# Kernel tuning notes

Hardware: AMD Instinct MI355X
Metric: run time of the kernel (lower is better)

The kernel has to match this reference:

```python
import jax, jax.numpy as jnp
import numpy as np

# T=timepoints, B=batch, N=neurons, H=lstm hidden, D=INPUT_DIM, P=len(PEOPLE)
T, B, N, H, D, P = 512, 64, 256, 64, 128, 64


def setup_inputs() -> dict:
    key = jax.random.key(0)
    ks = jax.random.split(key, 11)
    s = lambda k, shape, sc: jax.random.normal(k, shape, dtype=jnp.float32) * sc
    return {
        "input": s(ks[0], (T, B, D), 1.0),
        "W2n": s(ks[1], (N, D), D ** -0.5),      # linear2neurons weight [N, D]
        "b2n": s(ks[2], (N,), D ** -0.5),
        "W_ih": s(ks[3], (4 * H, 1), 1.0),        # LSTMCell input weights (input_size=1)
        "W_hh": s(ks[4], (4 * H, H), H ** -0.5),  # LSTMCell recurrent weights
        "b_ih": s(ks[5], (4 * H,), H ** -0.5),
        "b_hh": s(ks[6], (4 * H,), H ** -0.5),
        "Wg": s(ks[7], (1, H), H ** -0.5),        # linearLSTM: H -> 1 gain
        "bg": s(ks[8], (1,), H ** -0.5),
        "Wout": s(ks[9], (P, N), N ** -0.5),      # neurons2output
        "bout": s(ks[10], (P,), N ** -0.5),
    }


def reference(input, W2n, b2n, W_ih, W_hh, b_ih, b_hh, Wg, bg, Wout, bout):
    # Drive to every neuron for all timesteps: [T, B, N]
    x2n = jnp.einsum('tbd,nd->tbn', input, W2n) + b2n
    h0 = jnp.zeros((B, N, H), input.dtype)
    g0 = jnp.zeros((B, N), input.dtype)
    bias = b_ih + b_hh
    w_ih = W_ih[:, 0]  # [4H], since lstm input is scalar per neuron
    wg = Wg[0]         # [H]

    def step(carry, inp):
        h, c, g_prev1, g_prev2 = carry  # g_prev1 = g_{t-1}, g_prev2 = g_{t-2}
        xt, t = inp                     # xt: [B, N]
        # PyTorch LSTMCell gate order: i, f, g, o
        gates = xt[..., None] * w_ih + jnp.einsum('bnh,gh->bng', h, W_hh) + bias  # [B,N,4H]
        i_g, f_g, c_g, o_g = jnp.split(gates, 4, axis=-1)
        c = jax.nn.sigmoid(f_g) * c + jax.nn.sigmoid(i_g) * jnp.tanh(c_g)
        h = jax.nn.sigmoid(o_g) * jnp.tanh(c)
        g_t = jnp.einsum('bnh,h->bn', h, wg) + bg[0]  # gain at time t, [B,N]
        # original list semantics: t=0 uses g_t itself, t=1 uses constant 1, t>=2 uses g_{t-2}
        gain = jnp.where(t == 0, g_t, jnp.where(t == 1, jnp.ones_like(g_t), g_prev2))
        out = gain * jax.nn.softplus(xt - 1.0)  # log(1 + exp(x - 1))
        return (h, c, g_t, g_prev1), out

    _, out_neurons = jax.lax.scan(step, (h0, h0, g0, g0), (x2n, jnp.arange(T)))
    # out_neurons: [T, B, N] -> final projection to people logits [T, B, P]
    return jnp.einsum('tbn,pn->tbp', out_neurons, Wout) + bout
```

## Files before the change

### kernel.cpp

```cpp
#include <hip/hip_runtime.h>
#include <hip/hip_bf16.h>


typedef __attribute__((ext_vector_type(4))) float f32x4;
typedef __attribute__((ext_vector_type(4))) short s16x4;
typedef __attribute__((ext_vector_type(8))) short s16x8;
typedef __attribute__((ext_vector_type(4))) unsigned u32x4;

__device__ inline short bf16r(float f) {
    unsigned u = __builtin_bit_cast(unsigned, f);
    u += 0x7fffu + ((u >> 16) & 1u);
    return (short)(u >> 16);
}
__device__ inline float bf2f(short s) {
    unsigned u = ((unsigned)(unsigned short)s) << 16;
    return __builtin_bit_cast(float, u);
}
__device__ inline unsigned pkbf(float a, float b) {
    unsigned r;
    asm("v_cvt_pk_bf16_f32 %0, %1, %2" : "=v"(r) : "v"(a), "v"(b));
    return r;
}
__device__ inline f32x4 mfma32(s16x8 a, s16x8 b, f32x4 c) {
    return __builtin_amdgcn_mfma_f32_16x16x32_bf16(a, b, c, 0, 0, 0);
}

__global__ __launch_bounds__(256) void gemm_xwT(
    const float* __restrict__ X, const float* __restrict__ Wt,
    const float* __restrict__ bias, float* __restrict__ Out,
    int N, int K)
{
    __shared__ float Xs[32][68];
    __shared__ float Ws[32][68];
    const int tid = threadIdx.x;
    const int tx = tid & 15, ty = tid >> 4;
    const int m0 = blockIdx.x * 64, n0 = blockIdx.y * 64;
    const int kq = tid & 7, mr = tid >> 3;

    float acc[4][4];
#pragma unroll
    for (int i = 0; i < 4; ++i)
#pragma unroll
        for (int j = 0; j < 4; ++j) acc[i][j] = 0.f;

    for (int kc = 0; kc < K; kc += 32) {
#pragma unroll
        for (int rr = 0; rr < 2; ++rr) {
            const int m = mr + rr * 32;
            f32x4 xv = *(const f32x4*)(X + (size_t)(m0 + m) * K + kc + kq * 4);
            f32x4 wv = *(const f32x4*)(Wt + (size_t)(n0 + m) * K + kc + kq * 4);
#pragma unroll
            for (int j = 0; j < 4; ++j) { Xs[kq*4 + j][m] = xv[j]; Ws[kq*4 + j][m] = wv[j]; }
        }
        __syncthreads();
#pragma unroll
        for (int k = 0; k < 32; ++k) {
            f32x4 a = *(const f32x4*)&Xs[k][ty * 4];
            f32x4 b = *(const f32x4*)&Ws[k][tx * 4];
#pragma unroll
            for (int i = 0; i < 4; ++i)
#pragma unroll
                for (int j = 0; j < 4; ++j)
                    acc[i][j] = __builtin_fmaf(a[i], b[j], acc[i][j]);
        }
        __syncthreads();
    }
    f32x4 bv = *(const f32x4*)(bias + n0 + tx * 4);
#pragma unroll
    for (int i = 0; i < 4; ++i) {
        f32x4 o;
#pragma unroll
        for (int j = 0; j < 4; ++j) o[j] = acc[i][j] + bv[j];
        *(f32x4*)(Out + (size_t)(m0 + ty * 4 + i) * N + n0 + tx * 4) = o;
    }
}

__global__ __launch_bounds__(64, 1) void lstm_scan(
    const float* __restrict__ x2n,
    const float* __restrict__ W_hh,
    const float* __restrict__ w_ih,
    const float* __restrict__ b_ih,
    const float* __restrict__ b_hh,
    const float* __restrict__ wg,
    const float* __restrict__ bg,
    float* __restrict__ ON)
{
    const int lane = threadIdx.x & 63;
    const int c15 = lane & 15, g4 = lane >> 4;
    const int cellbase = blockIdx.x * 16;
    const float L2E = 1.4426950408889634f;

    s16x8 afw8[2][16];
    s16x8 afx8[16];
#pragma unroll
    for (int nt = 0; nt < 16; ++nt) {
        const float sc = ((nt >> 2) == 2) ? (2.f * L2E) : (-L2E);
        const float* wrow = W_hh + (size_t)(nt * 16 + c15) * 64;
#pragma unroll
        for (int kp = 0; kp < 2; ++kp) {
            s16x8 v;
#pragma unroll
            for (int half = 0; half < 2; ++half) {
                f32x4 w = *(const f32x4*)(wrow + (kp * 2 + half) * 16 + g4 * 4);
#pragma unroll
                for (int e = 0; e < 4; ++e) v[half * 4 + e] = bf16r(w[e] * sc);
            }
            afw8[kp][nt] = v;
        }
        const int g = nt * 16 + c15;
        const float wi = w_ih[g] * sc;
        const float bs = (b_ih[g] + b_hh[g]) * sc;
        const short wh = bf16r(wi);
        const short wl = bf16r(wi - bf2f(wh));
        const short bh_ = bf16r(bs);
        const short bl_ = bf16r(bs - bf2f(bh_));
        s16x8 v = (s16x8){0, 0, 0, 0, 0, 0, 0, 0};
        if (g4 == 0) { v[0] = wh; v[1] = wh; v[2] = wl; v[3] = bh_; }
        else if (g4 == 1) { v[0] = bl_; }
        afx8[nt] = v;
    }

    f32x4 wg_l[4];
#pragma unroll
    for (int q = 0; q < 4; ++q) wg_l[q] = *(const f32x4*)(wg + q * 16 + g4 * 4);
    const float bg0 = bg[0];
    const short one_bf = (short)0x3F80;

    f32x4 cst[4];
#pragma unroll
    for (int q = 0; q < 4; ++q) cst[q] = (f32x4){0.f, 0.f, 0.f, 0.f};
    s16x8 bh01 = (s16x8){0, 0, 0, 0, 0, 0, 0, 0};
    s16x8 bh23 = (s16x8){0, 0, 0, 0, 0, 0, 0, 0};

    float g_s1 = 0.f;
    float g2save = 0.f;
    float sp0 = 0.f;

    const size_t cellidx = (size_t)cellbase + c15;
    float xs0 = x2n[cellidx];
    float xs1 = x2n[(size_t)16384 + cellidx];

    for (int t = 0; t < 512; ++t) {
#pragma unroll
        for (int nt = 0; nt < 16; ++nt) {
            asm volatile("" : "+v"(afw8[0][nt]));
            asm volatile("" : "+v"(afw8[1][nt]));
            asm volatile("" : "+v"(afx8[nt]));
        }

        const float s2new = g_s1 + __shfl_xor(g_s1, 32, 64);

        const float xs_cur = xs0;
        xs0 = xs1;
        xs1 = x2n[(size_t)((t + 2) & 511) * 16384 + cellidx];

        const short xh = bf16r(xs_cur);
        const short xl = bf16r(xs_cur - bf2f(xh));
        s16x8 bx8 = (s16x8){0, 0, 0, 0, 0, 0, 0, 0};
        if (g4 == 0) { bx8[0] = xh; bx8[1] = xl; bx8[2] = xh; bx8[3] = one_bf; }
        else if (g4 == 1) { bx8[0] = one_bf; }

        unsigned bhw[8];
        float gpart = 0.f;
        const f32x4 zero4 = (f32x4){0.f, 0.f, 0.f, 0.f};
#pragma unroll
        for (int q = 0; q < 4; ++q) {
            f32x4 ai = mfma32(afx8[q], bx8, zero4);
            f32x4 af_ = mfma32(afx8[q + 4], bx8, zero4);
            f32x4 ag_ = mfma32(afx8[q + 8], bx8, zero4);
            f32x4 ao_ = mfma32(afx8[q + 12], bx8, zero4);
            ai  = mfma32(afw8[0][q], bh01, ai);       ai  = mfma32(afw8[1][q], bh23, ai);
            af_ = mfma32(afw8[0][q + 4], bh01, af_);  af_ = mfma32(afw8[1][q + 4], bh23, af_);
            ag_ = mfma32(afw8[0][q + 8], bh01, ag_);  ag_ = mfma32(afw8[1][q + 8], bh23, ag_);
            ao_ = mfma32(afw8[0][q + 12], bh01, ao_); ao_ = mfma32(afw8[1][q + 12], bh23, ao_);

            f32x4 hv;
#pragma unroll
            for (int ep = 0; ep < 2; ++ep) {
                const int ea = 2 * ep, eb = ea + 1;
                const float ufa = __builtin_amdgcn_exp2f(af_[ea]);
                const float ufb = __builtin_amdgcn_exp2f(af_[eb]);
                const float dfa = 1.f + ufa, dfb = 1.f + ufb;
                const float rf = __builtin_amdgcn_rcpf(dfa * dfb);
                const float sfa = rf * dfb, sfb = rf * dfa;

                const float uia = __builtin_amdgcn_exp2f(ai[ea]);
                const float uib = __builtin_amdgcn_exp2f(ai[eb]);
                const float vga = __builtin_amdgcn_exp2f(ag_[ea]);
                const float vgb = __builtin_amdgcn_exp2f(ag_[eb]);
                const float pa = (vga - 1.f) *
                    __builtin_amdgcn_rcpf((1.f + uia) * (1.f + vga));
                const float pb = (vgb - 1.f) *
                    __builtin_amdgcn_rcpf((1.f + uib) * (1.f + vgb));

                const float ca = __builtin_fmaf(sfa, cst[q][ea], pa);
                const float cb = __builtin_fmaf(sfb, cst[q][eb], pb);
                cst[q][ea] = ca; cst[q][eb] = cb;

                const float uoa = __builtin_amdgcn_exp2f(ao_[ea]);
                const float uob = __builtin_amdgcn_exp2f(ao_[eb]);
                const float vca = __builtin_amdgcn_exp2f(fminf(2.8853900817779268f * ca, 43.f));
                const float vcb = __builtin_amdgcn_exp2f(fminf(2.8853900817779268f * cb, 43.f));
                const float ha = (vca - 1.f) * __builtin_amdgcn_rcpf((1.f + uoa) * (1.f + vca));
                const float hb = (vcb - 1.f) * __builtin_amdgcn_rcpf((1.f + uob) * (1.f + vcb));
                hv[ea] = ha; hv[eb] = hb;
                bhw[q * 2 + ep] = pkbf(ha, hb);
            }
            gpart = __builtin_fmaf(hv[0], wg_l[q][0], gpart);
            gpart = __builtin_fmaf(hv[1], wg_l[q][1], gpart);
            gpart = __builtin_fmaf(hv[2], wg_l[q][2], gpart);
            gpart = __builtin_fmaf(hv[3], wg_l[q][3], gpart);
        }

        bh01 = __builtin_bit_cast(s16x8, (u32x4){bhw[0], bhw[1], bhw[2], bhw[3]});
        bh23 = __builtin_bit_cast(s16x8, (u32x4){bhw[4], bhw[5], bhw[6], bhw[7]});

        const float x1 = xs_cur - 1.f;
        const float sp = fmaxf(x1, 0.f) +
            0.6931471805599453f * __builtin_amdgcn_logf(
                1.f + __builtin_amdgcn_exp2f(-1.4426950408889634f * fabsf(x1)));
        if (t >= 2) {
            const float gain = g2save + bg0;
            if (g4 == 0) {
                ON[(size_t)t * 16384 + cellidx] = gain * sp;
                if (t == 2) ON[cellidx] = gain * sp0;
            }
        } else if (t == 1) {
            if (g4 == 0) ON[(size_t)16384 + cellidx] = sp;
        } else {
            sp0 = sp;
        }
        g2save = s2new;
        g_s1 = gpart + __shfl_xor(gpart, 16, 64);
    }
}

extern "C" void kernel_launch(void* const* d_in, const int* in_sizes, int n_in,
                              void* d_out, int out_size, void* d_ws, size_t ws_size,
                              hipStream_t stream)
{
    const float* input = (const float*)d_in[0];
    const float* W2n   = (const float*)d_in[1];
    const float* b2n   = (const float*)d_in[2];
    const float* W_ih  = (const float*)d_in[3];
    const float* W_hh  = (const float*)d_in[4];
    const float* b_ih  = (const float*)d_in[5];
    const float* b_hh  = (const float*)d_in[6];
    const float* Wg    = (const float*)d_in[7];
    const float* bg    = (const float*)d_in[8];
    const float* Wout  = (const float*)d_in[9];
    const float* bout  = (const float*)d_in[10];

    float* x2n = (float*)d_ws;
    float* ON  = x2n + (size_t)512 * 16384;

    gemm_xwT<<<dim3(512, 4), 256, 0, stream>>>(input, W2n, b2n, x2n, 256, 128);

    lstm_scan<<<1024, 64, 0, stream>>>(x2n, W_hh, W_ih, b_ih, b_hh, Wg, bg, ON);

    gemm_xwT<<<dim3(512, 1), 256, 0, stream>>>(ON, Wout, bout, (float*)d_out, 64, 256);
}
```

Before: 881.3 us.

## Software-pipeline LSTM step: precompute next input MFMA and split h into halves

The recurrent step is restructured so the input-projection MFMAs for step t+1 are issued up front into a second accumulator set, and the hidden-state MFMAs are issued in two halves. The first half runs as soon as the first two h tiles are ready, overlapping with the activation math for the second half. The loop is unrolled by two with ping-pong accumulators, and the asm register pins are removed. The intent is to shorten the serial critical path per timestep. The cost is more live VGPRs from the second 16-tile accumulator set, which risks spills at one wave per EU.

```diff
diff --git a/kernel.cpp b/kernel.cpp
--- a/kernel.cpp
+++ b/kernel.cpp
@@ -75,7 +75,146 @@
     }
 }
 
-__global__ __launch_bounds__(64, 1) void lstm_scan(
+__device__ __attribute__((always_inline)) inline void lstm_step(
+    const int t,
+    f32x4 (&acc)[16], f32x4 (&accn)[16],
+    const s16x8 (&afw8)[2][16], const s16x8 (&afx8)[16],
+    f32x4 (&cst)[4], const f32x4 (&wg_l)[4],
+    float& g_s1, float& g2save, float& sp0,
+    float& xs0, float& xs1,
+    const float bg0, const int g4, const size_t cellidx,
+    const float* __restrict__ x2n, float* __restrict__ ON)
+{
+    const float s2new = g_s1 + __shfl_xor(g_s1, 32, 64);
+
+    const float xs_cur = xs0;
+    const float xs_new = x2n[(size_t)((t + 2) & 511) * 16384 + cellidx];
+
+    const short one_bf = (short)0x3F80;
+    const short xh = bf16r(xs1);
+    const short xl = bf16r(xs1 - bf2f(xh));
+    s16x8 bx8 = (s16x8){0, 0, 0, 0, 0, 0, 0, 0};
+    if (g4 == 0) { bx8[0] = xh; bx8[1] = xl; bx8[2] = xh; bx8[3] = one_bf; }
+    else if (g4 == 1) { bx8[0] = one_bf; }
+    const f32x4 zero4 = (f32x4){0.f, 0.f, 0.f, 0.f};
+#pragma unroll
+    for (int nt = 0; nt < 16; ++nt) accn[nt] = mfma32(afx8[nt], bx8, zero4);
+
+    f32x4 hvf0, hvf1;
+    {
+        f32x4 cna, cnb, hna, hnb;
+#pragma unroll
+        for (int e = 0; e < 4; ++e) {
+            const float ufa = __builtin_amdgcn_exp2f(acc[4][e]);
+            const float ufb = __builtin_amdgcn_exp2f(acc[5][e]);
+            const float dfa = 1.f + ufa, dfb = 1.f + ufb;
+            const float rf = __builtin_amdgcn_rcpf(dfa * dfb);
+            const float sfa = rf * dfb, sfb = rf * dfa;
+
+            const float uia = __builtin_amdgcn_exp2f(acc[0][e]);
+            const float uib = __builtin_amdgcn_exp2f(acc[1][e]);
+            const float vga = __builtin_amdgcn_exp2f(acc[8][e]);
+            const float vgb = __builtin_amdgcn_exp2f(acc[9][e]);
+            const float pa = (vga - 1.f) *
+                __builtin_amdgcn_rcpf((1.f + uia) * (1.f + vga));
+            const float pb = (vgb - 1.f) *
+                __builtin_amdgcn_rcpf((1.f + uib) * (1.f + vgb));
+
+            const float ca = __builtin_fmaf(sfa, cst[0][e], pa);
+            const float cb = __builtin_fmaf(sfb, cst[1][e], pb);
+            cna[e] = ca; cnb[e] = cb;
+
+            const float uoa = __builtin_amdgcn_exp2f(acc[12][e]);
+            const float uob = __builtin_amdgcn_exp2f(acc[13][e]);
+            const float vca = __builtin_amdgcn_exp2f(fminf(2.8853900817779268f * ca, 43.f));
+            const float vcb = __builtin_amdgcn_exp2f(fminf(2.8853900817779268f * cb, 43.f));
+            hna[e] = (vca - 1.f) * __builtin_amdgcn_rcpf((1.f + uoa) * (1.f + vca));
+            hnb[e] = (vcb - 1.f) * __builtin_amdgcn_rcpf((1.f + uob) * (1.f + vcb));
+        }
+        cst[0] = cna; cst[1] = cnb;
+        hvf0 = hna; hvf1 = hnb;
+    }
+    const s16x8 bh01 = __builtin_bit_cast(s16x8,
+        (u32x4){pkbf(hvf0[0], hvf0[1]), pkbf(hvf0[2], hvf0[3]),
+                pkbf(hvf1[0], hvf1[1]), pkbf(hvf1[2], hvf1[3])});
+#pragma unroll
+    for (int nt = 0; nt < 16; ++nt) accn[nt] = mfma32(afw8[0][nt], bh01, accn[nt]);
+
+    f32x4 hvf2, hvf3;
+    {
+        f32x4 cna, cnb, hna, hnb;
+#pragma unroll
+        for (int e = 0; e < 4; ++e) {
+            const float ufa = __builtin_amdgcn_exp2f(acc[6][e]);
+            const float ufb = __builtin_amdgcn_exp2f(acc[7][e]);
+            const float dfa = 1.f + ufa, dfb = 1.f + ufb;
+            const float rf = __builtin_amdgcn_rcpf(dfa * dfb);
+            const float sfa = rf * dfb, sfb = rf * dfa;
+
+            const float uia = __builtin_amdgcn_exp2f(acc[2][e]);
+            const float uib = __builtin_amdgcn_exp2f(acc[3][e]);
+            const float vga = __builtin_amdgcn_exp2f(acc[10][e]);
+            const float vgb = __builtin_amdgcn_exp2f(acc[11][e]);
+            const float pa = (vga - 1.f) *
+                __builtin_amdgcn_rcpf((1.f + uia) * (1.f + vga));
+            const float pb = (vgb - 1.f) *
+                __builtin_amdgcn_rcpf((1.f + uib) * (1.f + vgb));
+
+            const float ca = __builtin_fmaf(sfa, cst[2][e], pa);
+            const float cb = __builtin_fmaf(sfb, cst[3][e], pb);
+            cna[e] = ca; cnb[e] = cb;
+
+            const float uoa = __builtin_amdgcn_exp2f(acc[14][e]);
+            const float uob = __builtin_amdgcn_exp2f(acc[15][e]);
+            const float vca = __builtin_amdgcn_exp2f(fminf(2.8853900817779268f * ca, 43.f));
+            const float vcb = __builtin_amdgcn_exp2f(fminf(2.8853900817779268f * cb, 43.f));
+            hna[e] = (vca - 1.f) * __builtin_amdgcn_rcpf((1.f + uoa) * (1.f + vca));
+            hnb[e] = (vcb - 1.f) * __builtin_amdgcn_rcpf((1.f + uob) * (1.f + vcb));
+        }
+        cst[2] = cna; cst[3] = cnb;
+        hvf2 = hna; hvf3 = hnb;
+    }
+    const s16x8 bh23 = __builtin_bit_cast(s16x8,
+        (u32x4){pkbf(hvf2[0], hvf2[1]), pkbf(hvf2[2], hvf2[3]),
+                pkbf(hvf3[0], hvf3[1]), pkbf(hvf3[2], hvf3[3])});
+#pragma unroll
+    for (int nt = 0; nt < 16; ++nt) accn[nt] = mfma32(afw8[1][nt], bh23, accn[nt]);
+
+    float gA = 0.f, gB = 0.f;
+#pragma unroll
+    for (int e = 0; e < 4; ++e) {
+        gA = __builtin_fmaf(hvf0[e], wg_l[0][e], gA);
+        gA = __builtin_fmaf(hvf1[e], wg_l[1][e], gA);
+        gB = __builtin_fmaf(hvf2[e], wg_l[2][e], gB);
+        gB = __builtin_fmaf(hvf3[e], wg_l[3][e], gB);
+    }
+    const float gpart = gA + gB;
+
+    const float x1 = xs_cur - 1.f;
+    const float sp = fmaxf(x1, 0.f) +
+        0.6931471805599453f * __builtin_amdgcn_logf(
+            1.f + __builtin_amdgcn_exp2f(-1.4426950408889634f * fabsf(x1)));
+    if (t >= 2) {
+        const float gain = g2save + bg0;
+        if (g4 == 0) {
+            ON[(size_t)t * 16384 + cellidx] = gain * sp;
+            if (t == 2) ON[cellidx] = gain * sp0;
+        }
+    } else if (t == 1) {
+        if (g4 == 0) ON[(size_t)16384 + cellidx] = sp;
+    } else {
+        sp0 = sp;
+    }
+    g2save = s2new;
+    g_s1 = gpart + __shfl_xor(gpart, 16, 64);
+    xs0 = xs1;
+    xs1 = xs_new;
+}
+
+__global__
+__attribute__((amdgpu_flat_work_group_size(64, 64)))
+__attribute__((amdgpu_waves_per_eu(1, 1)))
+void lstm_scan(
     const float* __restrict__ x2n,
     const float* __restrict__ W_hh,
     const float* __restrict__ w_ih,
@@ -124,114 +263,35 @@
 #pragma unroll
     for (int q = 0; q < 4; ++q) wg_l[q] = *(const f32x4*)(wg + q * 16 + g4 * 4);
     const float bg0 = bg[0];
-    const short one_bf = (short)0x3F80;
 
     f32x4 cst[4];
 #pragma unroll
     for (int q = 0; q < 4; ++q) cst[q] = (f32x4){0.f, 0.f, 0.f, 0.f};
-    s16x8 bh01 = (s16x8){0, 0, 0, 0, 0, 0, 0, 0};
-    s16x8 bh23 = (s16x8){0, 0, 0, 0, 0, 0, 0, 0};
-
-    float g_s1 = 0.f;
-    float g2save = 0.f;
-    float sp0 = 0.f;
+
+    float g_s1 = 0.f, g2save = 0.f, sp0 = 0.f;
 
     const size_t cellidx = (size_t)cellbase + c15;
     float xs0 = x2n[cellidx];
     float xs1 = x2n[(size_t)16384 + cellidx];
 
-    for (int t = 0; t < 512; ++t) {
-#pragma unroll
-        for (int nt = 0; nt < 16; ++nt) {
-            asm volatile("" : "+v"(afw8[0][nt]));
-            asm volatile("" : "+v"(afw8[1][nt]));
-            asm volatile("" : "+v"(afx8[nt]));
-        }
-
-        const float s2new = g_s1 + __shfl_xor(g_s1, 32, 64);
-
-        const float xs_cur = xs0;
-        xs0 = xs1;
-        xs1 = x2n[(size_t)((t + 2) & 511) * 16384 + cellidx];
-
-        const short xh = bf16r(xs_cur);
-        const short xl = bf16r(xs_cur - bf2f(xh));
+    f32x4 accA[16], accB[16];
+    {
+        const short one_bf = (short)0x3F80;
+        const short xh = bf16r(xs0);
+        const short xl = bf16r(xs0 - bf2f(xh));
         s16x8 bx8 = (s16x8){0, 0, 0, 0, 0, 0, 0, 0};
         if (g4 == 0) { bx8[0] = xh; bx8[1] = xl; bx8[2] = xh; bx8[3] = one_bf; }
         else if (g4 == 1) { bx8[0] = one_bf; }
-
-        unsigned bhw[8];
-        float gpart = 0.f;
         const f32x4 zero4 = (f32x4){0.f, 0.f, 0.f, 0.f};
 #pragma unroll
-        for (int q = 0; q < 4; ++q) {
-            f32x4 ai = mfma32(afx8[q], bx8, zero4);
-            f32x4 af_ = mfma32(afx8[q + 4], bx8, zero4);
-            f32x4 ag_ = mfma32(afx8[q + 8], bx8, zero4);
-            f32x4 ao_ = mfma32(afx8[q + 12], bx8, zero4);
-            ai  = mfma32(afw8[0][q], bh01, ai);       ai  = mfma32(afw8[1][q], bh23, ai);
-            af_ = mfma32(afw8[0][q + 4], bh01, af_);  af_ = mfma32(afw8[1][q + 4], bh23, af_);
-            ag_ = mfma32(afw8[0][q + 8], bh01, ag_);  ag_ = mfma32(afw8[1][q + 8], bh23, ag_);
-            ao_ = mfma32(afw8[0][q + 12], bh01, ao_); ao_ = mfma32(afw8[1][q + 12], bh23, ao_);
-
-            f32x4 hv;
-#pragma unroll
-            for (int ep = 0; ep < 2; ++ep) {
-                const int ea = 2 * ep, eb = ea + 1;
-                const float ufa = __builtin_amdgcn_exp2f(af_[ea]);
-                const float ufb = __builtin_amdgcn_exp2f(af_[eb]);
-                const float dfa = 1.f + ufa, dfb = 1.f + ufb;
-                const float rf = __builtin_amdgcn_rcpf(dfa * dfb);
-                const float sfa = rf * dfb, sfb = rf * dfa;
-
-                const float uia = __builtin_amdgcn_exp2f(ai[ea]);
-                const float uib = __builtin_amdgcn_exp2f(ai[eb]);
-                const float vga = __builtin_amdgcn_exp2f(ag_[ea]);
-                const float vgb = __builtin_amdgcn_exp2f(ag_[eb]);
-                const float pa = (vga - 1.f) *
-                    __builtin_amdgcn_rcpf((1.f + uia) * (1.f + vga));
-                const float pb = (vgb - 1.f) *
-                    __builtin_amdgcn_rcpf((1.f + uib) * (1.f + vgb));
-
-                const float ca = __builtin_fmaf(sfa, cst[q][ea], pa);
-                const float cb = __builtin_fmaf(sfb, cst[q][eb], pb);
-                cst[q][ea] = ca; cst[q][eb] = cb;
-
-                const float uoa = __builtin_amdgcn_exp2f(ao_[ea]);
-                const float uob = __builtin_amdgcn_exp2f(ao_[eb]);
-                const float vca = __builtin_amdgcn_exp2f(fminf(2.8853900817779268f * ca, 43.f));
-                const float vcb = __builtin_amdgcn_exp2f(fminf(2.8853900817779268f * cb, 43.f));
-                const float ha = (vca - 1.f) * __builtin_amdgcn_rcpf((1.f + uoa) * (1.f + vca));
-                const float hb = (vcb - 1.f) * __builtin_amdgcn_rcpf((1.f + uob) * (1.f + vcb));
-                hv[ea] = ha; hv[eb] = hb;
-                bhw[q * 2 + ep] = pkbf(ha, hb);
-            }
-            gpart = __builtin_fmaf(hv[0], wg_l[q][0], gpart);
-            gpart = __builtin_fmaf(hv[1], wg_l[q][1], gpart);
-            gpart = __builtin_fmaf(hv[2], wg_l[q][2], gpart);
-            gpart = __builtin_fmaf(hv[3], wg_l[q][3], gpart);
-        }
-
-        bh01 = __builtin_bit_cast(s16x8, (u32x4){bhw[0], bhw[1], bhw[2], bhw[3]});
-        bh23 = __builtin_bit_cast(s16x8, (u32x4){bhw[4], bhw[5], bhw[6], bhw[7]});
-
-        const float x1 = xs_cur - 1.f;
-        const float sp = fmaxf(x1, 0.f) +
-            0.6931471805599453f * __builtin_amdgcn_logf(
-                1.f + __builtin_amdgcn_exp2f(-1.4426950408889634f * fabsf(x1)));
-        if (t >= 2) {
-            const float gain = g2save + bg0;
-            if (g4 == 0) {
-                ON[(size_t)t * 16384 + cellidx] = gain * sp;
-                if (t == 2) ON[cellidx] = gain * sp0;
-            }
-        } else if (t == 1) {
-            if (g4 == 0) ON[(size_t)16384 + cellidx] = sp;
-        } else {
-            sp0 = sp;
-        }
-        g2save = s2new;
-        g_s1 = gpart + __shfl_xor(gpart, 16, 64);
+        for (int nt = 0; nt < 16; ++nt) accA[nt] = mfma32(afx8[nt], bx8, zero4);
+    }
+
+    for (int t = 0; t < 512; t += 2) {
+        lstm_step(t,     accA, accB, afw8, afx8, cst, wg_l,
+                  g_s1, g2save, sp0, xs0, xs1, bg0, g4, cellidx, x2n, ON);
+        lstm_step(t + 1, accB, accA, afw8, afx8, cst, wg_l,
+                  g_s1, g2save, sp0, xs0, xs1, bg0, g4, cellidx, x2n, ON);
     }
 }
 
```

Measured after the change: 834.4 us. -5.3%, faster.
